# Kernel tuning notes

Measured on AMD Instinct MI355X. Metric: run time of the kernel, lower is better.

Reference implementation:

```python
import jax, jax.numpy as jnp
import numpy as np

EMBED = 768
HEADS = 12
HEAD_DIM = EMBED // HEADS
HIDDEN = 3072
EPS = 1e-5


def setup_inputs() -> dict:
    key = jax.random.key(0)
    ks = jax.random.split(key, 8)
    s = lambda d: 1.0 / np.sqrt(d)
    return {
        "x": jax.random.normal(ks[0], (1, 4096, EMBED), jnp.float32),
        "ln1_w": jnp.ones((EMBED,), jnp.float32),
        "ln1_b": jnp.zeros((EMBED,), jnp.float32),
        "qkv_w": jax.random.normal(ks[1], (3 * EMBED, EMBED), jnp.float32) * s(EMBED),
        "qkv_b": jnp.zeros((3 * EMBED,), jnp.float32),
        "out_w": jax.random.normal(ks[2], (EMBED, EMBED), jnp.float32) * s(EMBED),
        "out_b": jnp.zeros((EMBED,), jnp.float32),
        "ln2_w": jnp.ones((EMBED,), jnp.float32),
        "ln2_b": jnp.zeros((EMBED,), jnp.float32),
        "fc1_w": jax.random.normal(ks[3], (HIDDEN, EMBED), jnp.float32) * s(EMBED),
        "fc1_b": jnp.zeros((HIDDEN,), jnp.float32),
        "fc2_w": jax.random.normal(ks[4], (EMBED, HIDDEN), jnp.float32) * s(HIDDEN),
        "fc2_b": jnp.zeros((EMBED,), jnp.float32),
    }


def _layernorm(x, w, b):
    mu = jnp.mean(x, axis=-1, keepdims=True)
    var = jnp.mean(jnp.square(x - mu), axis=-1, keepdims=True)
    return (x - mu) * jax.lax.rsqrt(var + EPS) * w + b


def reference(x, ln1_w, ln1_b, qkv_w, qkv_b, out_w, out_b,
              ln2_w, ln2_b, fc1_w, fc1_b, fc2_w, fc2_b):
    B, N, _ = x.shape
    # attention branch
    h = _layernorm(x, ln1_w, ln1_b)
    qkv = h @ qkv_w.T + qkv_b                      # [B,N,3E]
    qkv = qkv.reshape(B, N, 3, HEADS, HEAD_DIM)
    q = jnp.transpose(qkv[:, :, 0], (0, 2, 1, 3))  # [B,H,N,D]
    k = jnp.transpose(qkv[:, :, 1], (0, 2, 1, 3))
    v = jnp.transpose(qkv[:, :, 2], (0, 2, 1, 3))
    scores = jnp.einsum("bhqd,bhkd->bhqk", q, k) / np.sqrt(HEAD_DIM)
    probs = jax.nn.softmax(scores, axis=-1)
    attn = jnp.einsum("bhqk,bhkd->bhqd", probs, v)
    attn = jnp.transpose(attn, (0, 2, 1, 3)).reshape(B, N, EMBED)
    x = x + (attn @ out_w.T + out_b)
    # mlp branch
    h = _layernorm(x, ln2_w, ln2_b)
    h = jax.nn.gelu(h @ fc1_w.T + fc1_b, approximate=False)
    x = x + (h @ fc2_w.T + fc2_b)
    return x
```

## Files before the change

### kernel.cpp

```cpp
#include <hip/hip_runtime.h>
#include <hip/hip_bf16.h>

#define SEQ  4096
#define EMB  768
#define NH   12
#define HD   64
#define HID  3072
#define QKVC 2304

typedef __attribute__((ext_vector_type(8))) short bf16x8;
typedef __attribute__((ext_vector_type(4))) float f32x4;

#define MFMA16(a,b,c) __builtin_amdgcn_mfma_f32_16x16x32_bf16(a,b,c,0,0,0)

#define QSCL 0.18033688f
#define MFIX 16.0f

__device__ __forceinline__ unsigned short f2bf(float f){
  union { float f; unsigned u; } c; c.f = f;
  unsigned r = c.u + 0x7FFFu + ((c.u >> 16) & 1u);
  return (unsigned short)(r >> 16);
}

__device__ __forceinline__ float bf2f(unsigned short u){
  union { unsigned u; float f; } c; c.u = (unsigned)u << 16; return c.f;
}

__device__ __forceinline__ unsigned cvtpk(float a, float b){
  unsigned r;
  asm("v_cvt_pk_bf16_f32 %0, %1, %2" : "=v"(r) : "v"(a), "v"(b));
  return r;
}

__device__ __forceinline__ float gelu_f(float x){
  float x2 = x * x;
  float u  = __builtin_amdgcn_exp2f(x * fmaf(x2, 0.1029433f, 2.3022082f));
  return x * u * __builtin_amdgcn_rcpf(1.f + u);
}

__device__ __forceinline__ void gload_lds16(const unsigned short* g, unsigned short* l){
  __builtin_amdgcn_global_load_lds(
      (const __attribute__((address_space(1))) unsigned int*)g,
      (__attribute__((address_space(3))) unsigned int*)l, 16, 0, 0);
}

__global__ __launch_bounds__(256) void pre_kernel(
    const float* __restrict__ x, const float* __restrict__ w, const float* __restrict__ b,
    unsigned short* __restrict__ out,
    const float* __restrict__ s0, unsigned short* __restrict__ d0, int n0,
    const float* __restrict__ s1, unsigned short* __restrict__ d1, int n1,
    const float* __restrict__ s2, unsigned short* __restrict__ d2, int n2,
    const float* __restrict__ s3, unsigned short* __restrict__ d3, int n3)
{
  const int t = threadIdx.x;
  if (blockIdx.x < SEQ){
    const int row = blockIdx.x;
    const float* xr = x + (size_t)row * EMB;
    float v0 = xr[t], v1 = xr[t + 256], v2 = xr[t + 512];
    float s  = v0 + v1 + v2;
    float s2 = v0*v0 + v1*v1 + v2*v2;
    #pragma unroll
    for (int off = 32; off; off >>= 1){ s += __shfl_down(s, off); s2 += __shfl_down(s2, off); }
    __shared__ float rs[4], rq[4], st[2];
    int wv = t >> 6;
    if ((t & 63) == 0){ rs[wv] = s; rq[wv] = s2; }
    __syncthreads();
    if (t == 0){
      float S  = rs[0] + rs[1] + rs[2] + rs[3];
      float S2 = rq[0] + rq[1] + rq[2] + rq[3];
      float mu  = S * (1.f / 768.f);
      float var = S2 * (1.f / 768.f) - mu * mu;
      st[0] = mu; st[1] = rsqrtf(var + 1e-5f);
    }
    __syncthreads();
    float mu = st[0], rstd = st[1];
    unsigned short* orow = out + (size_t)row * EMB;
    orow[t]       = f2bf((v0 - mu) * rstd * w[t]       + b[t]);
    orow[t + 256] = f2bf((v1 - mu) * rstd * w[t + 256] + b[t + 256]);
    orow[t + 512] = f2bf((v2 - mu) * rstd * w[t + 512] + b[t + 512]);
  } else {
    long e = ((long)(blockIdx.x - SEQ) * 256 + t) << 2;
    const float* s; unsigned short* d;
    if (e < n0){ s = s0; d = d0; }
    else if ((e -= n0) < n1){ s = s1; d = d1; }
    else if ((e -= n1) < n2){ s = s2; d = d2; }
    else if ((e -= n2) < n3){ s = s3; d = d3; }
    else return;
    float4 v = *(const float4*)(s + e);
    ushort4 u;
    u.x = f2bf(v.x); u.y = f2bf(v.y); u.z = f2bf(v.z); u.w = f2bf(v.w);
    *(ushort4*)(d + e) = u;
  }
}

__global__ __launch_bounds__(256) void ln_kernel(const float* __restrict__ x,
    const float* __restrict__ w, const float* __restrict__ b,
    unsigned short* __restrict__ out)
{
  const int row = blockIdx.x;
  const float* xr = x + (size_t)row * EMB;
  const int t = threadIdx.x;
  float v0 = xr[t], v1 = xr[t + 256], v2 = xr[t + 512];
  float s  = v0 + v1 + v2;
  float s2 = v0*v0 + v1*v1 + v2*v2;
  #pragma unroll
  for (int off = 32; off; off >>= 1){ s += __shfl_down(s, off); s2 += __shfl_down(s2, off); }
  __shared__ float rs[4], rq[4], st[2];
  int wv = t >> 6;
  if ((t & 63) == 0){ rs[wv] = s; rq[wv] = s2; }
  __syncthreads();
  if (t == 0){
    float S  = rs[0] + rs[1] + rs[2] + rs[3];
    float S2 = rq[0] + rq[1] + rq[2] + rq[3];
    float mu  = S * (1.f / 768.f);
    float var = S2 * (1.f / 768.f) - mu * mu;
    st[0] = mu; st[1] = rsqrtf(var + 1e-5f);
  }
  __syncthreads();
  float mu = st[0], rstd = st[1];
  unsigned short* orow = out + (size_t)row * EMB;
  orow[t]       = f2bf((v0 - mu) * rstd * w[t]       + b[t]);
  orow[t + 256] = f2bf((v1 - mu) * rstd * w[t + 256] + b[t + 256]);
  orow[t + 512] = f2bf((v2 - mu) * rstd * w[t + 512] + b[t + 512]);
}

template<int EPI, int BM, int BN, int BK>
__global__ __launch_bounds__(256, 3) void gemm_kernel(
    const unsigned short* __restrict__ A, const unsigned short* __restrict__ B,
    const float* __restrict__ bias, const float* __restrict__ res,
    unsigned short* __restrict__ Ob, float* __restrict__ Of,
    int M, int N, int K)
{
  constexpr int MF  = BM / 32;
  constexpr int NF  = BN / 32;
  constexpr int KS  = BK / 32;
  constexpr int CPR = BK / 8;
  constexpr int AIT = BM * BK / 2048;
  constexpr int BIT = BN * BK / 2048;
  __shared__ unsigned short sA[3][BM * BK];
  __shared__ unsigned short sB[3][BN * BK];
  const int tid  = threadIdx.x;
  const int w    = tid >> 6, lane = tid & 63;
  const int wr   = w >> 1,   wc   = w & 1;
  const int l15  = lane & 15, l4  = lane >> 4;
  const int nb  = gridDim.x;
  const int lin = blockIdx.x;
  const int v   = (lin & 7) * (nb >> 3) + (lin >> 3);
  const int gN  = N / BN;
  const int tm  = v / gN, tn = v % gN;
  const unsigned short* Ab = A + (size_t)tm * BM * K;
  const unsigned short* Bb = B + (size_t)tn * BN * K;

  f32x4 acc[MF][NF];
  #pragma unroll
  for (int m = 0; m < MF; ++m)
    #pragma unroll
    for (int n = 0; n < NF; ++n){ acc[m][n][0]=0.f; acc[m][n][1]=0.f; acc[m][n][2]=0.f; acc[m][n][3]=0.f; }

  #define GSTAGE(buf, kt) { \
    const int k0_ = (kt) * BK; \
    _Pragma("unroll") \
    for (int i = 0; i < AIT; ++i){ \
      int c = i * 256 + tid; int row = c / CPR; int skc = (c % CPR) ^ (row & (CPR - 1)); \
      gload_lds16(Ab + (size_t)row * K + k0_ + skc * 8, &sA[buf][(i * 256 + w * 64) * 8]); } \
    _Pragma("unroll") \
    for (int i = 0; i < BIT; ++i){ \
      int c = i * 256 + tid; int row = c / CPR; int skc = (c % CPR) ^ (row & (CPR - 1)); \
      gload_lds16(Bb + (size_t)row * K + k0_ + skc * 8, &sB[buf][(i * 256 + w * 64) * 8]); }}

  #define GCOMPUTE(buf) { \
    _Pragma("unroll") \
    for (int ks = 0; ks < KS; ++ks){ \
      bf16x8 af[MF], bg[NF]; \
      _Pragma("unroll") \
      for (int m = 0; m < MF; ++m){ \
        int row = wr * (BM / 2) + m * 16 + l15; \
        int kc  = ks * 4 + l4; \
        af[m] = *(const bf16x8*)&sA[buf][row * BK + ((kc ^ (row & (CPR - 1))) << 3)]; } \
      _Pragma("unroll") \
      for (int n = 0; n < NF; ++n){ \
        int row = wc * (BN / 2) + n * 16 + l15; \
        int kc  = ks * 4 + l4; \
        bg[n] = *(const bf16x8*)&sB[buf][row * BK + ((kc ^ (row & (CPR - 1))) << 3)]; } \
      _Pragma("unroll") \
      for (int m = 0; m < MF; ++m) \
        _Pragma("unroll") \
        for (int n = 0; n < NF; ++n) \
          acc[m][n] = MFMA16(af[m], bg[n], acc[m][n]); }}

  const int nk = K / BK;
  GSTAGE(0, 0);
  GSTAGE(1, 1);
  for (int kt = 0; kt < nk; ++kt){
    if (kt + 2 < nk) asm volatile("s_waitcnt vmcnt(4)" ::: "memory");
    else             asm volatile("s_waitcnt vmcnt(0)" ::: "memory");
    __builtin_amdgcn_s_barrier();
    if (kt + 2 < nk) GSTAGE((kt + 2) % 3, kt + 2);
    GCOMPUTE(kt % 3);
  }
  #undef GSTAGE
  #undef GCOMPUTE

  #pragma unroll
  for (int m = 0; m < MF; ++m){
    int row0 = tm * BM + wr * (BM / 2) + m * 16 + l4 * 4;
    #pragma unroll
    for (int n = 0; n < NF; ++n){
      int col = tn * BN + wc * (BN / 2) + n * 16 + l15;
      float bv = bias[col];
      #pragma unroll
      for (int r = 0; r < 4; ++r){
        int row = row0 + r;
        float v2 = acc[m][n][r] + bv;
        if (EPI == 0){
          Ob[(size_t)row * N + col] = f2bf(v2);
        } else if (EPI == 1){
          Ob[(size_t)row * N + col] = f2bf(gelu_f(v2));
        } else if (EPI == 3){
          if (col < EMB) v2 *= QSCL;
          Ob[(size_t)row * N + col] = f2bf(v2);
        } else {
          v2 += res[(size_t)row * N + col];
          Of[(size_t)row * N + col] = v2;
        }
      }
    }
  }
}

__global__ __launch_bounds__(256, 3) void attn_kernel(
    const unsigned short* __restrict__ qkv,
    unsigned short* __restrict__ pO, float* __restrict__ pl)
{
  __shared__ unsigned short sK[2][64 * 64];
  __shared__ unsigned short sVt[2][64 * 64];
  __shared__ unsigned short sEp[4][16 * 72];
  const int tid = threadIdx.x, w = tid >> 6, lane = tid & 63;
  const int l15 = lane & 15, l4 = lane >> 4;

  const int bid  = blockIdx.x;
  const int v_id = (bid & 7) * 96 + (bid >> 3);
  const int head = v_id >> 6;
  const int r6   = v_id & 63;
  const int qt   = r6 >> 1;
  const int sk   = r6 & 1;

  const int koff = EMB + head * HD;
  const int voff = 2 * EMB + head * HD;
  const int qbase = qt * 128 + w * 32;
  const int tbase = sk * 32;

  bf16x8 qf[2][2];
  #pragma unroll
  for (int qg = 0; qg < 2; ++qg){
    const unsigned short* qp = qkv + (size_t)(qbase + qg * 16 + l15) * QKVC + head * HD + l4 * 8;
    qf[qg][0] = *(const bf16x8*)qp;
    qf[qg][1] = *(const bf16x8*)(qp + 32);
  }

  f32x4 oaccT[4][2];
  #pragma unroll
  for (int i = 0; i < 4; ++i)
    #pragma unroll
    for (int qg = 0; qg < 2; ++qg){ oaccT[i][qg][0]=0.f; oaccT[i][qg][1]=0.f; oaccT[i][qg][2]=0.f; oaccT[i][qg][3]=0.f; }
  float l0 = 0.f, l1 = 0.f;

  const int krow = tid >> 3;
  const int kskc = (tid & 7) ^ (krow & 7);
  const int vp_  = tid >> 3;
  const int d0   = (tid & 7) * 8;
  const int w16  = vp_ & 15;
  const int qpos = (w16 & 1) | (((w16 >> 3) & 1) << 1) | (((w16 >> 1) & 3) << 2);
  const int Pc   = ((vp_ >> 4) << 2) | (qpos >> 2);
  const int Ps   = qpos & 3;

  #define KSTAGE(buf, t) { \
    const int kv0_ = (t) << 6; \
    gload_lds16(qkv + (size_t)(kv0_ + krow) * QKVC + koff + kskc * 8,      &sK[buf][(w * 64) * 8]); \
    gload_lds16(qkv + (size_t)(kv0_ + 32 + krow) * QKVC + koff + kskc * 8, &sK[buf][(256 + w * 64) * 8]); }

  #define VLOAD(t) { \
    const unsigned short* vp = qkv + (size_t)(((t) << 6) + vp_ * 2) * QKVC + voff + d0; \
    va = *(const bf16x8*)vp; \
    vb = *(const bf16x8*)(vp + QKVC); }

  #define VCOMMIT(buf) { \
    _Pragma("unroll") \
    for (int i = 0; i < 8; ++i){ \
      unsigned pk = (unsigned)(unsigned short)va[i] | ((unsigned)(unsigned short)vb[i] << 16); \
      *(unsigned*)&sVt[buf][(d0 + i) * 64 + ((Pc ^ (tid & 7) ^ i) << 3) + Ps * 2] = pk; \
    } }

  bf16x8 va, vb;
  KSTAGE(0, tbase);
  VLOAD(tbase);
  VCOMMIT(0);

  for (int tt = 0; tt < 32; ++tt){
    const int cur = tt & 1;
    __syncthreads();
    const bool pre = (tt < 31);
    if (pre){
      KSTAGE(cur ^ 1, tbase + tt + 1);
      VLOAD(tbase + tt + 1);
    }

    f32x4 sf[4][2];
    #pragma unroll
    for (int i = 0; i < 4; ++i)
      #pragma unroll
      for (int qg = 0; qg < 2; ++qg){ sf[i][qg][0]=0.f; sf[i][qg][1]=0.f; sf[i][qg][2]=0.f; sf[i][qg][3]=0.f; }
    __builtin_amdgcn_s_setprio(1);
    #pragma unroll
    for (int ks = 0; ks < 2; ++ks){
      bf16x8 kf[4];
      #pragma unroll
      for (int nb = 0; nb < 4; ++nb){
        int row = 16 * nb + l15;
        kf[nb] = *(const bf16x8*)&sK[cur][(row * 8 + ((4 * ks + l4) ^ (row & 7))) * 8];
      }
      #pragma unroll
      for (int nb = 0; nb < 4; ++nb){
        sf[nb][0] = MFMA16(kf[nb], qf[0][ks], sf[nb][0]);
        sf[nb][1] = MFMA16(kf[nb], qf[1][ks], sf[nb][1]);
      }
    }
    __builtin_amdgcn_s_setprio(0);

    unsigned pbw[2][2][4];
    {
      float ps0 = 0.f, ps1 = 0.f;
      #pragma unroll
      for (int nb = 0; nb < 4; ++nb){
        float p0[4], p1[4];
        #pragma unroll
        for (int r = 0; r < 4; ++r){
          p0[r] = __builtin_amdgcn_exp2f(sf[nb][0][r] - MFIX); ps0 += p0[r];
          p1[r] = __builtin_amdgcn_exp2f(sf[nb][1][r] - MFIX); ps1 += p1[r];
        }
        pbw[0][nb >> 1][(nb & 1) * 2]     = cvtpk(p0[0], p0[1]);
        pbw[0][nb >> 1][(nb & 1) * 2 + 1] = cvtpk(p0[2], p0[3]);
        pbw[1][nb >> 1][(nb & 1) * 2]     = cvtpk(p1[0], p1[1]);
        pbw[1][nb >> 1][(nb & 1) * 2 + 1] = cvtpk(p1[2], p1[3]);
      }
      ps0 += __shfl_xor(ps0, 16); ps0 += __shfl_xor(ps0, 32);
      ps1 += __shfl_xor(ps1, 16); ps1 += __shfl_xor(ps1, 32);
      l0 += ps0; l1 += ps1;
    }

    __builtin_amdgcn_s_setprio(1);
    {
      bf16x8 vv[2][4];
      #pragma unroll
      for (int ks = 0; ks < 2; ++ks)
        #pragma unroll
        for (int db = 0; db < 4; ++db){
          int d = 16 * db + l15;
          int cp = (4 * ks + l4) ^ ((d >> 3) & 7) ^ (d & 7);
          vv[ks][db] = *(const bf16x8*)&sVt[cur][d * 64 + cp * 8];
        }
      union { unsigned uw[4]; bf16x8 v; } pb;
      #pragma unroll
      for (int qg = 0; qg < 2; ++qg){
        bf16x8 pb0, pb1;
        pb.uw[0]=pbw[qg][0][0]; pb.uw[1]=pbw[qg][0][1]; pb.uw[2]=pbw[qg][0][2]; pb.uw[3]=pbw[qg][0][3]; pb0 = pb.v;
        pb.uw[0]=pbw[qg][1][0]; pb.uw[1]=pbw[qg][1][1]; pb.uw[2]=pbw[qg][1][2]; pb.uw[3]=pbw[qg][1][3]; pb1 = pb.v;
        #pragma unroll
        for (int db = 0; db < 4; ++db){
          oaccT[db][qg] = MFMA16(vv[0][db], pb0, oaccT[db][qg]);
          oaccT[db][qg] = MFMA16(vv[1][db], pb1, oaccT[db][qg]);
        }
      }
    }
    __builtin_amdgcn_s_setprio(0);

    if (pre) VCOMMIT(cur ^ 1);
  }

  #pragma unroll
  for (int qg = 0; qg < 2; ++qg){
    unsigned short* sPw = sEp[w];
    #pragma unroll
    for (int db = 0; db < 4; ++db)
      #pragma unroll
      for (int dw = 0; dw < 2; ++dw){
        unsigned pk = cvtpk(oaccT[db][qg][2 * dw], oaccT[db][qg][2 * dw + 1]);
        *(unsigned*)&sPw[l15 * 72 + 16 * db + 4 * l4 + 2 * dw] = pk;
      }
    int qe = lane >> 2, de = (lane & 3) * 16;
    bf16x8 r0 = *(const bf16x8*)&sPw[qe * 72 + de];
    bf16x8 r1 = *(const bf16x8*)&sPw[qe * 72 + de + 8];
    unsigned short* op = pO + ((size_t)(sk * NH + head) * SEQ + qbase + qg * 16 + qe) * 64 + de;
    *(bf16x8*)op = r0;
    *(bf16x8*)(op + 8) = r1;
  }
  if (lane < 16){
    size_t r = (size_t)(sk * NH + head) * SEQ + qbase + l15;
    pl[r]      = l0;
    pl[r + 16] = l1;
  }
  #undef KSTAGE
  #undef VLOAD
  #undef VCOMMIT
}

__global__ __launch_bounds__(256) void comb_kernel(
    const unsigned short* __restrict__ pO, const float* __restrict__ pl,
    unsigned short* __restrict__ o)
{
  const int t = threadIdx.x;
  const int row = blockIdx.x * 64 + (t >> 2);
  const int dseg = (t & 3) * 16;
  float inv = 1.f / (pl[row] + pl[NH * SEQ + row]);
  const unsigned short* p0 = pO + (size_t)row * 64 + dseg;
  const unsigned short* p1 = p0 + (size_t)NH * SEQ * 64;
  bf16x8 x0 = *(const bf16x8*)p0, x1 = *(const bf16x8*)(p0 + 8);
  bf16x8 y0 = *(const bf16x8*)p1, y1 = *(const bf16x8*)(p1 + 8);
  const int head = row >> 12, q = row & (SEQ - 1);
  unsigned short* op = o + (size_t)q * EMB + head * HD + dseg;
  union { unsigned uw[4]; bf16x8 v; } r0, r1;
  #pragma unroll
  for (int i = 0; i < 4; ++i){
    r0.uw[i] = cvtpk(inv * (bf2f((unsigned short)x0[2*i])   + bf2f((unsigned short)y0[2*i])),
                     inv * (bf2f((unsigned short)x0[2*i+1]) + bf2f((unsigned short)y0[2*i+1])));
    r1.uw[i] = cvtpk(inv * (bf2f((unsigned short)x1[2*i])   + bf2f((unsigned short)y1[2*i])),
                     inv * (bf2f((unsigned short)x1[2*i+1]) + bf2f((unsigned short)y1[2*i+1])));
  }
  *(bf16x8*)op = r0.v;
  *(bf16x8*)(op + 8) = r1.v;
}

extern "C" void kernel_launch(void* const* d_in, const int* in_sizes, int n_in,
                              void* d_out, int out_size, void* d_ws, size_t ws_size,
                              hipStream_t stream)
{
  const float* x    = (const float*)d_in[0];
  const float* ln1w = (const float*)d_in[1];
  const float* ln1b = (const float*)d_in[2];
  const float* qkvw = (const float*)d_in[3];
  const float* qkvb = (const float*)d_in[4];
  const float* outw = (const float*)d_in[5];
  const float* outb = (const float*)d_in[6];
  const float* ln2w = (const float*)d_in[7];
  const float* ln2b = (const float*)d_in[8];
  const float* fc1w = (const float*)d_in[9];
  const float* fc1b = (const float*)d_in[10];
  const float* fc2w = (const float*)d_in[11];
  const float* fc2b = (const float*)d_in[12];
  float* out = (float*)d_out;

  char* ws = (char*)d_ws;
  unsigned short* wqkv = (unsigned short*)ws; ws += (size_t)QKVC * EMB * 2;
  unsigned short* wout = (unsigned short*)ws; ws += (size_t)EMB * EMB * 2;
  unsigned short* wfc1 = (unsigned short*)ws; ws += (size_t)HID * EMB * 2;
  unsigned short* wfc2 = (unsigned short*)ws; ws += (size_t)EMB * HID * 2;
  unsigned short* h1   = (unsigned short*)ws; ws += (size_t)SEQ * EMB * 2;
  unsigned short* qkv  = (unsigned short*)ws; ws += (size_t)SEQ * QKVC * 2;
  unsigned short* h3   = (unsigned short*)ws; ws += (size_t)SEQ * HID * 2;
  unsigned short* attnb = h1;
  unsigned short* h2    = qkv;
  unsigned short* pO  = h3;
  float*          pl  = (float*)(h3 + (size_t)2 * NH * SEQ * 64);

  const int n0 = QKVC * EMB, n1 = EMB * EMB, n2 = HID * EMB, n3 = EMB * HID;
  pre_kernel<<<SEQ + (n0 + n1 + n2 + n3) / 4 / 256, 256, 0, stream>>>(
      x, ln1w, ln1b, h1,
      qkvw, wqkv, n0, outw, wout, n1, fc1w, wfc1, n2, fc2w, wfc2, n3);

  gemm_kernel<3, 128, 128, 32><<<(SEQ / 128) * (QKVC / 128), 256, 0, stream>>>(
      h1, wqkv, qkvb, nullptr, qkv, nullptr, SEQ, QKVC, EMB);

  attn_kernel<<<SEQ / 128 * NH * 2, 256, 0, stream>>>(qkv, pO, pl);
  comb_kernel<<<NH * SEQ / 64, 256, 0, stream>>>(pO, pl, attnb);

  gemm_kernel<2, 64, 64, 64><<<(SEQ / 64) * (EMB / 64), 256, 0, stream>>>(
      attnb, wout, outb, x, nullptr, out, SEQ, EMB, EMB);

  ln_kernel<<<SEQ, 256, 0, stream>>>(out, ln2w, ln2b, h2);

  gemm_kernel<1, 128, 128, 32><<<(SEQ / 128) * (HID / 128), 256, 0, stream>>>(
      h2, wfc1, fc1b, nullptr, h3, nullptr, SEQ, HID, EMB);

  gemm_kernel<2, 64, 64, 64><<<(SEQ / 64) * (EMB / 64), 256, 0, stream>>>(
      h3, wfc2, fc2b, out, nullptr, out, SEQ, EMB, HID);
}
```

Measured before the change: 197.7 us.

## Fuse split-KV attention combine into output projection GEMM A-operand load

Removes the separate combine kernel that merged the two split-K attention partials and normalized by the summed softmax denominators. The output-projection GEMM now reads both partials and the l values directly, normalizes and converts them to bf16 in registers, and writes them to LDS as its A tile. This saves one launch and the write and re-read of the intermediate attention buffer. The cost is that each N-tile block redoes the combine work (12 tiles along N) and reads twice as many A bytes.

```diff
diff --git a/kernel.cpp b/kernel.cpp
--- a/kernel.cpp
+++ b/kernel.cpp
@@ -228,6 +228,125 @@
   }
 }
 
+__global__ __launch_bounds__(256, 3) void gemm_op_kernel(
+    const unsigned short* __restrict__ pO, const float* __restrict__ pl,
+    const unsigned short* __restrict__ B, const float* __restrict__ bias,
+    const float* __restrict__ res, float* __restrict__ Of)
+{
+  __shared__ unsigned short sA[2][64 * 64];
+  __shared__ unsigned short sB[2][64 * 64];
+  const int tid  = threadIdx.x;
+  const int w    = tid >> 6, lane = tid & 63;
+  const int wr   = w >> 1,   wc   = w & 1;
+  const int l15  = lane & 15, l4  = lane >> 4;
+  const int nb  = gridDim.x;
+  const int lin = blockIdx.x;
+  const int v   = (lin & 7) * (nb >> 3) + (lin >> 3);
+  const int gN  = EMB / 64;
+  const int tm  = v / gN, tn = v % gN;
+  const unsigned short* Bb = B + (size_t)tn * 64 * EMB;
+
+  f32x4 acc[2][2];
+  #pragma unroll
+  for (int m = 0; m < 2; ++m)
+    #pragma unroll
+    for (int n = 0; n < 2; ++n){ acc[m][n][0]=0.f; acc[m][n][1]=0.f; acc[m][n][2]=0.f; acc[m][n][3]=0.f; }
+
+  const int arow = tid >> 3;
+  const int askc = (tid & 7) ^ (arow & 7);
+  const int q0 = tm * 64 + arow, q1 = q0 + 32;
+  const size_t SK1 = (size_t)NH * SEQ * 64;
+
+  bf16x8 a00, a01, a10, a11;
+  float lt0, lt1;
+
+  #define ALOAD(t) { \
+    const unsigned short* pa = pO + ((size_t)(t) * SEQ + q0) * 64 + askc * 8; \
+    const unsigned short* pb_ = pO + ((size_t)(t) * SEQ + q1) * 64 + askc * 8; \
+    a00 = *(const bf16x8*)pa;  a01 = *(const bf16x8*)(pa + SK1); \
+    a10 = *(const bf16x8*)pb_; a11 = *(const bf16x8*)(pb_ + SK1); \
+    lt0 = pl[(size_t)(t) * SEQ + q0] + pl[(size_t)(NH + (t)) * SEQ + q0]; \
+    lt1 = pl[(size_t)(t) * SEQ + q1] + pl[(size_t)(NH + (t)) * SEQ + q1]; }
+
+  #define ACOMMIT(buf) { \
+    float i0 = 1.f / lt0, i1 = 1.f / lt1; \
+    union { unsigned uw[4]; bf16x8 v; } u0, u1; \
+    _Pragma("unroll") \
+    for (int j = 0; j < 4; ++j){ \
+      u0.uw[j] = cvtpk((bf2f((unsigned short)a00[2*j])   + bf2f((unsigned short)a01[2*j]))   * i0, \
+                       (bf2f((unsigned short)a00[2*j+1]) + bf2f((unsigned short)a01[2*j+1])) * i0); \
+      u1.uw[j] = cvtpk((bf2f((unsigned short)a10[2*j])   + bf2f((unsigned short)a11[2*j]))   * i1, \
+                       (bf2f((unsigned short)a10[2*j+1]) + bf2f((unsigned short)a11[2*j+1])) * i1); \
+    } \
+    *(bf16x8*)&sA[buf][tid * 8]         = u0.v; \
+    *(bf16x8*)&sA[buf][(256 + tid) * 8] = u1.v; }
+
+  #define BSTAGE(buf, kt) { \
+    const int k0_ = (kt) * 64; \
+    _Pragma("unroll") \
+    for (int i = 0; i < 2; ++i){ \
+      int c = i * 256 + tid; int row = c >> 3; int skc = (c & 7) ^ (row & 7); \
+      gload_lds16(Bb + (size_t)row * EMB + k0_ + skc * 8, &sB[buf][(i * 256 + w * 64) * 8]); }}
+
+  #define OCOMPUTE(buf) { \
+    _Pragma("unroll") \
+    for (int ks = 0; ks < 2; ++ks){ \
+      bf16x8 af[2], bg[2]; \
+      _Pragma("unroll") \
+      for (int m = 0; m < 2; ++m){ \
+        int row = wr * 32 + m * 16 + l15; \
+        int kc  = ks * 4 + l4; \
+        af[m] = *(const bf16x8*)&sA[buf][row * 64 + ((kc ^ (row & 7)) << 3)]; } \
+      _Pragma("unroll") \
+      for (int n = 0; n < 2; ++n){ \
+        int row = wc * 32 + n * 16 + l15; \
+        int kc  = ks * 4 + l4; \
+        bg[n] = *(const bf16x8*)&sB[buf][row * 64 + ((kc ^ (row & 7)) << 3)]; } \
+      _Pragma("unroll") \
+      for (int m = 0; m < 2; ++m) \
+        _Pragma("unroll") \
+        for (int n = 0; n < 2; ++n) \
+          acc[m][n] = MFMA16(af[m], bg[n], acc[m][n]); }}
+
+  ALOAD(0);
+  BSTAGE(0, 0);
+  ACOMMIT(0);
+  __syncthreads();
+
+  int cur = 0;
+  for (int kt = 0; kt < NH; ++kt){
+    const bool pre = (kt + 1 < NH);
+    if (pre){
+      ALOAD(kt + 1);
+      BSTAGE(cur ^ 1, kt + 1);
+    }
+    OCOMPUTE(cur);
+    if (pre) ACOMMIT(cur ^ 1);
+    __syncthreads();
+    cur ^= 1;
+  }
+  #undef ALOAD
+  #undef ACOMMIT
+  #undef BSTAGE
+  #undef OCOMPUTE
+
+  #pragma unroll
+  for (int m = 0; m < 2; ++m){
+    int row0 = tm * 64 + wr * 32 + m * 16 + l4 * 4;
+    #pragma unroll
+    for (int n = 0; n < 2; ++n){
+      int col = tn * 64 + wc * 32 + n * 16 + l15;
+      float bv = bias[col];
+      #pragma unroll
+      for (int r = 0; r < 4; ++r){
+        int row = row0 + r;
+        float v2 = acc[m][n][r] + bv + res[(size_t)row * EMB + col];
+        Of[(size_t)row * EMB + col] = v2;
+      }
+    }
+  }
+}
+
 __global__ __launch_bounds__(256, 3) void attn_kernel(
     const unsigned short* __restrict__ qkv,
     unsigned short* __restrict__ pO, float* __restrict__ pl)
@@ -402,32 +521,6 @@
   #undef KSTAGE
   #undef VLOAD
   #undef VCOMMIT
-}
-
-__global__ __launch_bounds__(256) void comb_kernel(
-    const unsigned short* __restrict__ pO, const float* __restrict__ pl,
-    unsigned short* __restrict__ o)
-{
-  const int t = threadIdx.x;
-  const int row = blockIdx.x * 64 + (t >> 2);
-  const int dseg = (t & 3) * 16;
-  float inv = 1.f / (pl[row] + pl[NH * SEQ + row]);
-  const unsigned short* p0 = pO + (size_t)row * 64 + dseg;
-  const unsigned short* p1 = p0 + (size_t)NH * SEQ * 64;
-  bf16x8 x0 = *(const bf16x8*)p0, x1 = *(const bf16x8*)(p0 + 8);
-  bf16x8 y0 = *(const bf16x8*)p1, y1 = *(const bf16x8*)(p1 + 8);
-  const int head = row >> 12, q = row & (SEQ - 1);
-  unsigned short* op = o + (size_t)q * EMB + head * HD + dseg;
-  union { unsigned uw[4]; bf16x8 v; } r0, r1;
-  #pragma unroll
-  for (int i = 0; i < 4; ++i){
-    r0.uw[i] = cvtpk(inv * (bf2f((unsigned short)x0[2*i])   + bf2f((unsigned short)y0[2*i])),
-                     inv * (bf2f((unsigned short)x0[2*i+1]) + bf2f((unsigned short)y0[2*i+1])));
-    r1.uw[i] = cvtpk(inv * (bf2f((unsigned short)x1[2*i])   + bf2f((unsigned short)y1[2*i])),
-                     inv * (bf2f((unsigned short)x1[2*i+1]) + bf2f((unsigned short)y1[2*i+1])));
-  }
-  *(bf16x8*)op = r0.v;
-  *(bf16x8*)(op + 8) = r1.v;
 }
 
 extern "C" void kernel_launch(void* const* d_in, const int* in_sizes, int n_in,
@@ -457,7 +550,6 @@
   unsigned short* h1   = (unsigned short*)ws; ws += (size_t)SEQ * EMB * 2;
   unsigned short* qkv  = (unsigned short*)ws; ws += (size_t)SEQ * QKVC * 2;
   unsigned short* h3   = (unsigned short*)ws; ws += (size_t)SEQ * HID * 2;
-  unsigned short* attnb = h1;
   unsigned short* h2    = qkv;
   unsigned short* pO  = h3;
   float*          pl  = (float*)(h3 + (size_t)2 * NH * SEQ * 64);
@@ -471,10 +563,9 @@
       h1, wqkv, qkvb, nullptr, qkv, nullptr, SEQ, QKVC, EMB);
 
   attn_kernel<<<SEQ / 128 * NH * 2, 256, 0, stream>>>(qkv, pO, pl);
-  comb_kernel<<<NH * SEQ / 64, 256, 0, stream>>>(pO, pl, attnb);
-
-  gemm_kernel<2, 64, 64, 64><<<(SEQ / 64) * (EMB / 64), 256, 0, stream>>>(
-      attnb, wout, outb, x, nullptr, out, SEQ, EMB, EMB);
+
+  gemm_op_kernel<<<(SEQ / 64) * (EMB / 64), 256, 0, stream>>>(
+      pO, pl, wout, outb, x, out);
 
   ln_kernel<<<SEQ, 256, 0, stream>>>(out, ln2w, ln2b, h2);
 
```

Measured after the change: 199.1 us. No clear change (+0.7%).
